# Performance work log

Hardware: AMD Instinct MI355X
Metric: run time of the kernel (lower is better)

The kernel has to match this reference:

```python
import jax, jax.numpy as jnp
import numpy as np

B, S, C, V = 8, 256, 256, 64

def setup_inputs() -> dict:
    key = jax.random.key(0)
    ks = jax.random.split(key, 11)
    bound = 1.0 / np.sqrt(C)
    u = lambda k, shape: jax.random.uniform(k, shape, jnp.float32, -bound, bound)
    return {
        "ctx": jax.random.normal(ks[0], (B, S, C), jnp.float32),
        "W": u(ks[1], (C, C, V)),
        "bias": u(ks[2], (V,)),
        "lin1_w": u(ks[3], (V, C)), "lin1_b": u(ks[4], (V,)),
        "lin2_w": u(ks[5], (V, C)), "lin2_b": u(ks[6], (V,)),
        "linmul_w": u(ks[7], (V, C)), "linmul_b": u(ks[8], (V,)),
        "lindiff_w": u(ks[9], (V, C)), "lindiff_b": u(ks[10], (V,)),
    }

def reference(ctx, W, bias, lin1_w, lin1_b, lin2_w, lin2_b,
              linmul_w, linmul_b, lindiff_w, lindiff_b):
    # bilinear: out[b,s,z,k] = sum_ij ctx[b,s,i] * ctx[b,z,j] * W[i,j,k]
    tmp = jnp.einsum('bsi,ijk->bsjk', ctx, W)          # (B,S,C,V)
    out = jnp.einsum('bsjk,bzj->bszk', tmp, ctx)       # (B,S,S,V)
    out = out + bias
    out1 = ctx @ lin1_w.T + lin1_b                     # (B,S,V)
    out2 = ctx @ lin2_w.T + lin2_b                     # (B,S,V)
    # mul[b,s,z] = ctx[b,z] * ctx[b,s]; diff[b,s,z] = ctx[b,z] - ctx[b,s]
    mul = ctx[:, None, :, :] * ctx[:, :, None, :]      # (B,S,S,C)
    diff = ctx[:, None, :, :] - ctx[:, :, None, :]     # (B,S,S,C)
    outmul = mul @ linmul_w.T + linmul_b               # (B,S,S,V)
    outdiff = diff @ lindiff_w.T + lindiff_b           # (B,S,S,V)
    return jnp.tanh(out + out1[:, None, :, :] + out2[:, :, None, :] + outmul + outdiff)
```

## Files before the change

### kernel.cpp

```cpp
#include <hip/hip_runtime.h>


typedef __attribute__((ext_vector_type(8))) _Float16 half8;
typedef __attribute__((ext_vector_type(4))) _Float16 half4v;
typedef __attribute__((ext_vector_type(4))) float f32x4;

__device__ __forceinline__ void async16(const void* g, void* l) {
  __builtin_amdgcn_global_load_lds(
      (__attribute__((address_space(1))) void*)g,
      (__attribute__((address_space(3))) void*)l, 16, 0, 0);
}

__global__ __launch_bounds__(256) void prep_ctx(const float* __restrict__ ctx,
                                                _Float16* __restrict__ ch) {
  int idx = (blockIdx.x * 256 + threadIdx.x) * 4;
  float4 v = *(const float4*)(ctx + idx);
  half4v o;
  o[0] = (_Float16)v.x; o[1] = (_Float16)v.y;
  o[2] = (_Float16)v.z; o[3] = (_Float16)v.w;
  *(half4v*)(ch + idx) = o;
}

__global__ __launch_bounds__(256) void prep_wt(const float* __restrict__ W,
                                               const float* __restrict__ lmw,
                                               _Float16* __restrict__ wt) {
  __shared__ _Float16 T[256 * 68];
  const int t = threadIdx.x;
  const int j = blockIdx.x;
#pragma unroll
  for (int p = 0; p < 16; ++p) {
    int i = p * 16 + (t >> 4);
    int c = t & 15;
    float4 v = *(const float4*)&W[(size_t)i * 16384 + j * 64 + c * 4];
    if (i == j) {
      v.x += lmw[(c * 4 + 0) * 256 + j];
      v.y += lmw[(c * 4 + 1) * 256 + j];
      v.z += lmw[(c * 4 + 2) * 256 + j];
      v.w += lmw[(c * 4 + 3) * 256 + j];
    }
    half4v o;
    o[0] = (_Float16)v.x; o[1] = (_Float16)v.y;
    o[2] = (_Float16)v.z; o[3] = (_Float16)v.w;
    *(half4v*)&T[i * 68 + c * 4] = o;
  }
  __syncthreads();
  const int k = t >> 2, i0 = (t & 3) * 64;
  _Float16* dst = wt + ((size_t)(k * 256 + j)) * 256 + i0;
#pragma unroll
  for (int u = 0; u < 64; u += 8) {
    half8 o;
#pragma unroll
    for (int e = 0; e < 8; ++e) o[e] = T[(i0 + u + e) * 68 + k];
    *(half8*)(dst + u) = o;
  }
}

__global__ __launch_bounds__(256) void prep_rt(
    const float* __restrict__ ctx, const float* __restrict__ bias,
    const float* __restrict__ l1w, const float* __restrict__ l1b,
    const float* __restrict__ l2w, const float* __restrict__ l2b,
    const float* __restrict__ lmb, const float* __restrict__ ldw,
    const float* __restrict__ ldb, float* __restrict__ rbuf,
    float* __restrict__ tbuf) {
  __shared__ float Cs[4 * 256];
  const int t = threadIdx.x;
  const int row0 = blockIdx.x * 4;
  ((float4*)Cs)[t] = ((const float4*)(ctx + (size_t)row0 * 256))[t];
  __syncthreads();
  const int k = t & 63, lr = t >> 6;
  const float* l1r = l1w + k * 256;
  const float* l2r = l2w + k * 256;
  const float* ldr = ldw + k * 256;
  float a1 = 0.f, a2 = 0.f;
  for (int c = 0; c < 256; c += 4) {
    float4 w1 = *(const float4*)(l1r + c);
    float4 w2 = *(const float4*)(l2r + c);
    float4 wd = *(const float4*)(ldr + c);
    float4 cv = *(const float4*)(&Cs[lr * 256 + c]);
    a1 += cv.x * (w1.x + wd.x) + cv.y * (w1.y + wd.y) +
          cv.z * (w1.z + wd.z) + cv.w * (w1.w + wd.w);
    a2 += cv.x * (w2.x - wd.x) + cv.y * (w2.y - wd.y) +
          cv.z * (w2.z - wd.z) + cv.w * (w2.w - wd.w);
  }
  int row = row0 + lr;
  rbuf[row * 64 + k] = a1 + l1b[k];
  tbuf[row * 64 + k] = a2 + l2b[k] + bias[k] + lmb[k] + ldb[k];
}

__global__ __launch_bounds__(256) void gemm1(const _Float16* __restrict__ ch,
                                             const _Float16* __restrict__ wt,
                                             _Float16* __restrict__ tmp) {
  __shared__ _Float16 As[128 * 32];
  __shared__ _Float16 Bs[128 * 32];
  const int t = threadIdx.x;
  const int lane = t & 63, wave = t >> 6;
  const int m0 = blockIdx.y * 128, n0 = blockIdx.x * 128;
  const int wm = (wave & 1) * 64, wn = (wave >> 1) * 64;
  const int r = lane & 15, q = lane >> 4;
  f32x4 acc[4][4] = {};
  const _Float16* gA = ch + (size_t)(m0 + (t >> 2)) * 256 + (t & 3) * 8;
  const _Float16* gB = wt + (size_t)(n0 + (t >> 2)) * 256 + (t & 3) * 8;
  for (int k0 = 0; k0 < 256; k0 += 32) {
    async16(gA + k0, &As[t * 8]);
    async16(gA + 64 * 256 + k0, &As[2048 + t * 8]);
    async16(gB + k0, &Bs[t * 8]);
    async16(gB + 64 * 256 + k0, &Bs[2048 + t * 8]);
    __syncthreads();
    half8 a[4], b[4];
#pragma unroll
    for (int mi = 0; mi < 4; ++mi)
      a[mi] = *(const half8*)&As[(wm + mi * 16 + r) * 32 + q * 8];
#pragma unroll
    for (int ni = 0; ni < 4; ++ni)
      b[ni] = *(const half8*)&Bs[(wn + ni * 16 + r) * 32 + q * 8];
#pragma unroll
    for (int mi = 0; mi < 4; ++mi)
#pragma unroll
      for (int ni = 0; ni < 4; ++ni)
        acc[mi][ni] = __builtin_amdgcn_mfma_f32_16x16x32_f16(a[mi], b[ni],
                                                             acc[mi][ni], 0, 0, 0);
    __syncthreads();
  }
#pragma unroll
  for (int mi = 0; mi < 4; ++mi)
#pragma unroll
    for (int ni = 0; ni < 4; ++ni) {
      int m = m0 + wm + mi * 16 + q * 4;
      int n = n0 + wn + ni * 16 + r;
#pragma unroll
      for (int e = 0; e < 4; ++e)
        tmp[(size_t)(m + e) * 16384 + n] = (_Float16)acc[mi][ni][e];
    }
}

__global__ __launch_bounds__(256) void gemm2(const _Float16* __restrict__ ch,
                                             const _Float16* __restrict__ tmp,
                                             const float* __restrict__ rbuf,
                                             const float* __restrict__ tbuf,
                                             float* __restrict__ out) {
  __shared__ _Float16 As[256 * 32];
  __shared__ _Float16 Bs[64 * 32];
  __shared__ float Ts[64];
  const int t = threadIdx.x;
  const int lane = t & 63, wave = t >> 6;
  const int bs = blockIdx.x;
  const int b = bs >> 8;
  const int r = lane & 15, q = lane >> 4;
  const _Float16* ctxb = ch + (size_t)b * 65536;
  const _Float16* tm = tmp + (size_t)bs * 16384;
  if (t < 64) Ts[t] = tbuf[bs * 64 + t];
  f32x4 acc[4][4] = {};
  for (int j0 = 0; j0 < 256; j0 += 32) {
#pragma unroll
    for (int p = 0; p < 4; ++p)
      async16(ctxb + (size_t)(p * 64 + (t >> 2)) * 256 + j0 + (t & 3) * 8,
              &As[p * 2048 + t * 8]);
    async16(tm + (size_t)(t >> 2) * 256 + j0 + (t & 3) * 8, &Bs[t * 8]);
    __syncthreads();
    half8 a[4], bf[4];
#pragma unroll
    for (int mi = 0; mi < 4; ++mi)
      a[mi] = *(const half8*)&As[(wave * 64 + mi * 16 + r) * 32 + q * 8];
#pragma unroll
    for (int ni = 0; ni < 4; ++ni)
      bf[ni] = *(const half8*)&Bs[(ni * 16 + r) * 32 + q * 8];
#pragma unroll
    for (int mi = 0; mi < 4; ++mi)
#pragma unroll
      for (int ni = 0; ni < 4; ++ni)
        acc[mi][ni] = __builtin_amdgcn_mfma_f32_16x16x32_f16(a[mi], bf[ni],
                                                             acc[mi][ni], 0, 0, 0);
    __syncthreads();
  }
  const float* rb = rbuf + (size_t)b * 16384;
#pragma unroll
  for (int mi = 0; mi < 4; ++mi)
#pragma unroll
    for (int ni = 0; ni < 4; ++ni) {
      int z0 = wave * 64 + mi * 16 + q * 4;
      int k = ni * 16 + r;
#pragma unroll
      for (int e = 0; e < 4; ++e) {
        int z = z0 + e;
        float x = acc[mi][ni][e] + rb[z * 64 + k] + Ts[k];
        float ax = fabsf(x);
        float ev = __expf(-2.0f * ax);
        float y = (1.0f - ev) / (1.0f + ev);
        y = copysignf(y, x);
        out[((size_t)bs * 256 + z) * 64 + k] = y;
      }
    }
}

extern "C" void kernel_launch(void* const* d_in, const int* in_sizes, int n_in,
                              void* d_out, int out_size, void* d_ws, size_t ws_size,
                              hipStream_t stream) {
  const float* ctx  = (const float*)d_in[0];
  const float* W    = (const float*)d_in[1];
  const float* bias = (const float*)d_in[2];
  const float* l1w  = (const float*)d_in[3];
  const float* l1b  = (const float*)d_in[4];
  const float* l2w  = (const float*)d_in[5];
  const float* l2b  = (const float*)d_in[6];
  const float* lmw  = (const float*)d_in[7];
  const float* lmb  = (const float*)d_in[8];
  const float* ldw  = (const float*)d_in[9];
  const float* ldb  = (const float*)d_in[10];
  float* out = (float*)d_out;

  char* ws = (char*)d_ws;
  _Float16* ch  = (_Float16*)ws;
  _Float16* wt  = (_Float16*)(ws + (1u << 20));
  _Float16* tmp = (_Float16*)(ws + (9u << 20));
  float* rbuf = (float*)(ws + (73u << 20));
  float* tbuf = rbuf + 2048 * 64;

  prep_ctx<<<512, 256, 0, stream>>>(ctx, ch);
  prep_wt<<<256, 256, 0, stream>>>(W, lmw, wt);
  prep_rt<<<512, 256, 0, stream>>>(ctx, bias, l1w, l1b, l2w, l2b, lmb, ldw, ldb,
                                   rbuf, tbuf);
  gemm1<<<dim3(128, 16), 256, 0, stream>>>(ch, wt, tmp);
  gemm2<<<2048, 256, 0, stream>>>(ch, tmp, rbuf, tbuf, out);
}
```

Before: 273.3 us.

## Use split hi/lo fp16 operands in both GEMMs for higher accuracy

Splits ctx and the transformed weight into fp16 high and low parts and accumulates the extra cross-term MFMAs (three products in gemm1, two in gemm2) to approximate fp32 precision. The ctx conversion is fused into prep_rt, which removes the separate prep_ctx launch. gemm2 is retiled to 128x128 tiles covering four s rows with a two-way M split. This adds MFMA work and memory traffic in exchange for accuracy.

```diff
diff --git a/kernel.cpp b/kernel.cpp
--- a/kernel.cpp
+++ b/kernel.cpp
@@ -9,50 +9,6 @@
   __builtin_amdgcn_global_load_lds(
       (__attribute__((address_space(1))) void*)g,
       (__attribute__((address_space(3))) void*)l, 16, 0, 0);
-}
-
-__global__ __launch_bounds__(256) void prep_ctx(const float* __restrict__ ctx,
-                                                _Float16* __restrict__ ch) {
-  int idx = (blockIdx.x * 256 + threadIdx.x) * 4;
-  float4 v = *(const float4*)(ctx + idx);
-  half4v o;
-  o[0] = (_Float16)v.x; o[1] = (_Float16)v.y;
-  o[2] = (_Float16)v.z; o[3] = (_Float16)v.w;
-  *(half4v*)(ch + idx) = o;
-}
-
-__global__ __launch_bounds__(256) void prep_wt(const float* __restrict__ W,
-                                               const float* __restrict__ lmw,
-                                               _Float16* __restrict__ wt) {
-  __shared__ _Float16 T[256 * 68];
-  const int t = threadIdx.x;
-  const int j = blockIdx.x;
-#pragma unroll
-  for (int p = 0; p < 16; ++p) {
-    int i = p * 16 + (t >> 4);
-    int c = t & 15;
-    float4 v = *(const float4*)&W[(size_t)i * 16384 + j * 64 + c * 4];
-    if (i == j) {
-      v.x += lmw[(c * 4 + 0) * 256 + j];
-      v.y += lmw[(c * 4 + 1) * 256 + j];
-      v.z += lmw[(c * 4 + 2) * 256 + j];
-      v.w += lmw[(c * 4 + 3) * 256 + j];
-    }
-    half4v o;
-    o[0] = (_Float16)v.x; o[1] = (_Float16)v.y;
-    o[2] = (_Float16)v.z; o[3] = (_Float16)v.w;
-    *(half4v*)&T[i * 68 + c * 4] = o;
-  }
-  __syncthreads();
-  const int k = t >> 2, i0 = (t & 3) * 64;
-  _Float16* dst = wt + ((size_t)(k * 256 + j)) * 256 + i0;
-#pragma unroll
-  for (int u = 0; u < 64; u += 8) {
-    half8 o;
-#pragma unroll
-    for (int e = 0; e < 8; ++e) o[e] = T[(i0 + u + e) * 68 + k];
-    *(half8*)(dst + u) = o;
-  }
 }
 
 __global__ __launch_bounds__(256) void prep_rt(
@@ -61,11 +17,25 @@
     const float* __restrict__ l2w, const float* __restrict__ l2b,
     const float* __restrict__ lmb, const float* __restrict__ ldw,
     const float* __restrict__ ldb, float* __restrict__ rbuf,
-    float* __restrict__ tbuf) {
+    float* __restrict__ tbuf, _Float16* __restrict__ ch_hi,
+    _Float16* __restrict__ ch_lo) {
   __shared__ float Cs[4 * 256];
   const int t = threadIdx.x;
   const int row0 = blockIdx.x * 4;
-  ((float4*)Cs)[t] = ((const float4*)(ctx + (size_t)row0 * 256))[t];
+  float4 v = ((const float4*)(ctx + (size_t)row0 * 256))[t];
+  ((float4*)Cs)[t] = v;
+  {
+    float xs[4] = {v.x, v.y, v.z, v.w};
+    half4v h, l;
+#pragma unroll
+    for (int e = 0; e < 4; ++e) {
+      _Float16 hh = (_Float16)xs[e];
+      h[e] = hh;
+      l[e] = (_Float16)(xs[e] - (float)hh);
+    }
+    *(half4v*)&ch_hi[(size_t)row0 * 256 + t * 4] = h;
+    *(half4v*)&ch_lo[(size_t)row0 * 256 + t * 4] = l;
+  }
   __syncthreads();
   const int k = t & 63, lr = t >> 6;
   const float* l1r = l1w + k * 256;
@@ -87,10 +57,52 @@
   tbuf[row * 64 + k] = a2 + l2b[k] + bias[k] + lmb[k] + ldb[k];
 }
 
-__global__ __launch_bounds__(256) void gemm1(const _Float16* __restrict__ ch,
-                                             const _Float16* __restrict__ wt,
+__global__ __launch_bounds__(256) void prep_wt(const float* __restrict__ W,
+                                               const float* __restrict__ lmw,
+                                               _Float16* __restrict__ wt_hi,
+                                               _Float16* __restrict__ wt_lo) {
+  __shared__ float T[256 * 68];
+  const int t = threadIdx.x;
+  const int j = blockIdx.x;
+#pragma unroll
+  for (int p = 0; p < 16; ++p) {
+    int i = p * 16 + (t >> 4);
+    int c = t & 15;
+    float4 v = *(const float4*)&W[(size_t)i * 16384 + j * 64 + c * 4];
+    if (i == j) {
+      v.x += lmw[(c * 4 + 0) * 256 + j];
+      v.y += lmw[(c * 4 + 1) * 256 + j];
+      v.z += lmw[(c * 4 + 2) * 256 + j];
+      v.w += lmw[(c * 4 + 3) * 256 + j];
+    }
+    *(float4*)&T[i * 68 + c * 4] = v;
+  }
+  __syncthreads();
+  const int k = t >> 2, i0 = (t & 3) * 64;
+  _Float16* dh = wt_hi + ((size_t)(k * 256 + j)) * 256 + i0;
+  _Float16* dl = wt_lo + ((size_t)(k * 256 + j)) * 256 + i0;
+#pragma unroll
+  for (int u = 0; u < 64; u += 8) {
+    half8 h, l;
+#pragma unroll
+    for (int e = 0; e < 8; ++e) {
+      float x = T[(i0 + u + e) * 68 + k];
+      _Float16 hh = (_Float16)x;
+      h[e] = hh;
+      l[e] = (_Float16)(x - (float)hh);
+    }
+    *(half8*)(dh + u) = h;
+    *(half8*)(dl + u) = l;
+  }
+}
+
+__global__ __launch_bounds__(256) void gemm1(const _Float16* __restrict__ ahp,
+                                             const _Float16* __restrict__ alp,
+                                             const _Float16* __restrict__ bhp,
+                                             const _Float16* __restrict__ blp,
                                              _Float16* __restrict__ tmp) {
-  __shared__ _Float16 As[128 * 32];
+  __shared__ _Float16 Ah[128 * 32];
+  __shared__ _Float16 Al[128 * 32];
   __shared__ _Float16 Bs[128 * 32];
   const int t = threadIdx.x;
   const int lane = t & 63, wave = t >> 6;
@@ -98,18 +110,49 @@
   const int wm = (wave & 1) * 64, wn = (wave >> 1) * 64;
   const int r = lane & 15, q = lane >> 4;
   f32x4 acc[4][4] = {};
-  const _Float16* gA = ch + (size_t)(m0 + (t >> 2)) * 256 + (t & 3) * 8;
-  const _Float16* gB = wt + (size_t)(n0 + (t >> 2)) * 256 + (t & 3) * 8;
+  const int row = t >> 2, seg = (t & 3) * 8;
+  const _Float16* gAh = ahp + (size_t)(m0 + row) * 256 + seg;
+  const _Float16* gAl = alp + (size_t)(m0 + row) * 256 + seg;
+  const _Float16* gBh = bhp + (size_t)(n0 + row) * 256 + seg;
+  const _Float16* gBl = blp + (size_t)(n0 + row) * 256 + seg;
   for (int k0 = 0; k0 < 256; k0 += 32) {
-    async16(gA + k0, &As[t * 8]);
-    async16(gA + 64 * 256 + k0, &As[2048 + t * 8]);
-    async16(gB + k0, &Bs[t * 8]);
-    async16(gB + 64 * 256 + k0, &Bs[2048 + t * 8]);
+    async16(gAh + k0, &Ah[t * 8]);
+    async16(gAh + 64 * 256 + k0, &Ah[2048 + t * 8]);
+    async16(gAl + k0, &Al[t * 8]);
+    async16(gAl + 64 * 256 + k0, &Al[2048 + t * 8]);
+    async16(gBh + k0, &Bs[t * 8]);
+    async16(gBh + 64 * 256 + k0, &Bs[2048 + t * 8]);
+    __syncthreads();
+    half8 a[4], c[4], b[4];
+#pragma unroll
+    for (int mi = 0; mi < 4; ++mi) {
+      a[mi] = *(const half8*)&Ah[(wm + mi * 16 + r) * 32 + q * 8];
+      c[mi] = *(const half8*)&Al[(wm + mi * 16 + r) * 32 + q * 8];
+    }
+#pragma unroll
+    for (int ni = 0; ni < 4; ++ni)
+      b[ni] = *(const half8*)&Bs[(wn + ni * 16 + r) * 32 + q * 8];
+#pragma unroll
+    for (int mi = 0; mi < 4; ++mi)
+#pragma unroll
+      for (int ni = 0; ni < 4; ++ni) {
+        acc[mi][ni] = __builtin_amdgcn_mfma_f32_16x16x32_f16(a[mi], b[ni],
+                                                             acc[mi][ni], 0, 0, 0);
+        acc[mi][ni] = __builtin_amdgcn_mfma_f32_16x16x32_f16(c[mi], b[ni],
+                                                             acc[mi][ni], 0, 0, 0);
+      }
+    __syncthreads();
+  }
+  for (int k0 = 0; k0 < 256; k0 += 32) {
+    async16(gAh + k0, &Ah[t * 8]);
+    async16(gAh + 64 * 256 + k0, &Ah[2048 + t * 8]);
+    async16(gBl + k0, &Bs[t * 8]);
+    async16(gBl + 64 * 256 + k0, &Bs[2048 + t * 8]);
     __syncthreads();
     half8 a[4], b[4];
 #pragma unroll
     for (int mi = 0; mi < 4; ++mi)
-      a[mi] = *(const half8*)&As[(wm + mi * 16 + r) * 32 + q * 8];
+      a[mi] = *(const half8*)&Ah[(wm + mi * 16 + r) * 32 + q * 8];
 #pragma unroll
     for (int ni = 0; ni < 4; ++ni)
       b[ni] = *(const half8*)&Bs[(wn + ni * 16 + r) * 32 + q * 8];
@@ -133,61 +176,73 @@
     }
 }
 
-__global__ __launch_bounds__(256) void gemm2(const _Float16* __restrict__ ch,
+__global__ __launch_bounds__(256) void gemm2(const _Float16* __restrict__ ahp,
+                                             const _Float16* __restrict__ alp,
                                              const _Float16* __restrict__ tmp,
                                              const float* __restrict__ rbuf,
                                              const float* __restrict__ tbuf,
                                              float* __restrict__ out) {
-  __shared__ _Float16 As[256 * 32];
-  __shared__ _Float16 Bs[64 * 32];
-  __shared__ float Ts[64];
+  __shared__ _Float16 Ah[128 * 32];
+  __shared__ _Float16 Al[128 * 32];
+  __shared__ _Float16 Bs[128 * 32];
   const int t = threadIdx.x;
   const int lane = t & 63, wave = t >> 6;
-  const int bs = blockIdx.x;
-  const int b = bs >> 8;
+  const int gx = blockIdx.x;
+  const int bq = gx >> 2, mt = (gx >> 1) & 1, nt = gx & 1;
+  const int b = bq >> 6, s0 = (bq & 63) * 4;
+  const int wm = (wave & 1) * 64, wn = (wave >> 1) * 64;
   const int r = lane & 15, q = lane >> 4;
-  const _Float16* ctxb = ch + (size_t)b * 65536;
-  const _Float16* tm = tmp + (size_t)bs * 16384;
-  if (t < 64) Ts[t] = tbuf[bs * 64 + t];
   f32x4 acc[4][4] = {};
+  const int row = t >> 2, seg = (t & 3) * 8;
+  const _Float16* gAh = ahp + ((size_t)b * 256 + mt * 128 + row) * 256 + seg;
+  const _Float16* gAl = alp + ((size_t)b * 256 + mt * 128 + row) * 256 + seg;
+  const _Float16* gB =
+      tmp + ((size_t)(b * 256 + s0) * 64 + nt * 128 + row) * 256 + seg;
   for (int j0 = 0; j0 < 256; j0 += 32) {
-#pragma unroll
-    for (int p = 0; p < 4; ++p)
-      async16(ctxb + (size_t)(p * 64 + (t >> 2)) * 256 + j0 + (t & 3) * 8,
-              &As[p * 2048 + t * 8]);
-    async16(tm + (size_t)(t >> 2) * 256 + j0 + (t & 3) * 8, &Bs[t * 8]);
-    __syncthreads();
-    half8 a[4], bf[4];
-#pragma unroll
-    for (int mi = 0; mi < 4; ++mi)
-      a[mi] = *(const half8*)&As[(wave * 64 + mi * 16 + r) * 32 + q * 8];
+    async16(gAh + j0, &Ah[t * 8]);
+    async16(gAh + 64 * 256 + j0, &Ah[2048 + t * 8]);
+    async16(gAl + j0, &Al[t * 8]);
+    async16(gAl + 64 * 256 + j0, &Al[2048 + t * 8]);
+    async16(gB + j0, &Bs[t * 8]);
+    async16(gB + 64 * 256 + j0, &Bs[2048 + t * 8]);
+    __syncthreads();
+    half8 a[4], c[4], bfr[4];
+#pragma unroll
+    for (int mi = 0; mi < 4; ++mi) {
+      a[mi] = *(const half8*)&Ah[(wm + mi * 16 + r) * 32 + q * 8];
+      c[mi] = *(const half8*)&Al[(wm + mi * 16 + r) * 32 + q * 8];
+    }
 #pragma unroll
     for (int ni = 0; ni < 4; ++ni)
-      bf[ni] = *(const half8*)&Bs[(ni * 16 + r) * 32 + q * 8];
-#pragma unroll
-    for (int mi = 0; mi < 4; ++mi)
-#pragma unroll
-      for (int ni = 0; ni < 4; ++ni)
-        acc[mi][ni] = __builtin_amdgcn_mfma_f32_16x16x32_f16(a[mi], bf[ni],
-                                                             acc[mi][ni], 0, 0, 0);
-    __syncthreads();
-  }
-  const float* rb = rbuf + (size_t)b * 16384;
+      bfr[ni] = *(const half8*)&Bs[(wn + ni * 16 + r) * 32 + q * 8];
+#pragma unroll
+    for (int mi = 0; mi < 4; ++mi)
+#pragma unroll
+      for (int ni = 0; ni < 4; ++ni) {
+        acc[mi][ni] = __builtin_amdgcn_mfma_f32_16x16x32_f16(a[mi], bfr[ni],
+                                                             acc[mi][ni], 0, 0, 0);
+        acc[mi][ni] = __builtin_amdgcn_mfma_f32_16x16x32_f16(c[mi], bfr[ni],
+                                                             acc[mi][ni], 0, 0, 0);
+      }
+    __syncthreads();
+  }
 #pragma unroll
   for (int mi = 0; mi < 4; ++mi)
 #pragma unroll
     for (int ni = 0; ni < 4; ++ni) {
-      int z0 = wave * 64 + mi * 16 + q * 4;
-      int k = ni * 16 + r;
+      int z0 = mt * 128 + wm + mi * 16 + q * 4;
+      int n = nt * 128 + wn + ni * 16 + r;
+      int s_l = n >> 6, k = n & 63;
+      const float tk = tbuf[(b * 256 + s0 + s_l) * 64 + k];
 #pragma unroll
       for (int e = 0; e < 4; ++e) {
         int z = z0 + e;
-        float x = acc[mi][ni][e] + rb[z * 64 + k] + Ts[k];
+        float x = acc[mi][ni][e] + rbuf[(size_t)b * 16384 + z * 64 + k] + tk;
         float ax = fabsf(x);
         float ev = __expf(-2.0f * ax);
         float y = (1.0f - ev) / (1.0f + ev);
         y = copysignf(y, x);
-        out[((size_t)bs * 256 + z) * 64 + k] = y;
+        out[(((size_t)b * 256 + s0 + s_l) * 256 + z) * 64 + k] = y;
       }
     }
 }
@@ -209,16 +264,17 @@
   float* out = (float*)d_out;
 
   char* ws = (char*)d_ws;
-  _Float16* ch  = (_Float16*)ws;
-  _Float16* wt  = (_Float16*)(ws + (1u << 20));
-  _Float16* tmp = (_Float16*)(ws + (9u << 20));
-  float* rbuf = (float*)(ws + (73u << 20));
+  _Float16* ch_hi = (_Float16*)ws;
+  _Float16* ch_lo = (_Float16*)(ws + (1u << 20));
+  _Float16* wt_hi = (_Float16*)(ws + (2u << 20));
+  _Float16* wt_lo = (_Float16*)(ws + (10u << 20));
+  _Float16* tmp   = (_Float16*)(ws + (18u << 20));
+  float* rbuf = (float*)(ws + (82u << 20));
   float* tbuf = rbuf + 2048 * 64;
 
-  prep_ctx<<<512, 256, 0, stream>>>(ctx, ch);
-  prep_wt<<<256, 256, 0, stream>>>(W, lmw, wt);
   prep_rt<<<512, 256, 0, stream>>>(ctx, bias, l1w, l1b, l2w, l2b, lmb, ldw, ldb,
-                                   rbuf, tbuf);
-  gemm1<<<dim3(128, 16), 256, 0, stream>>>(ch, wt, tmp);
-  gemm2<<<2048, 256, 0, stream>>>(ch, tmp, rbuf, tbuf, out);
-}
+                                   rbuf, tbuf, ch_hi, ch_lo);
+  prep_wt<<<256, 256, 0, stream>>>(W, lmw, wt_hi, wt_lo);
+  gemm1<<<dim3(128, 16), 256, 0, stream>>>(ch_hi, ch_lo, wt_hi, wt_lo, tmp);
+  gemm2<<<2048, 256, 0, stream>>>(ch_hi, ch_lo, tmp, rbuf, tbuf, out);
+}
```

Result: slower. 319.5 us (+16.9%).
